# Kernel optimization log

Measured on AMD Instinct MI355X. Metric: run time of the kernel, lower is better.

Reference implementation:

```python
import jax, jax.numpy as jnp
import numpy as np

N = 200000   # nodes
E = 6400000  # directed edges (avg degree 32)
F = 128      # num_features
C = 16       # num_classes
H1, H2, H3 = 4, 4, 2  # hardcoded GCN hidden dims from the source


def setup_inputs():
    key = jax.random.key(0)
    ks = jax.random.split(key, 10)
    x = jax.random.normal(ks[0], (N, F), dtype=jnp.float32)
    edge_index = jax.random.randint(ks[1], (2, E), 0, N, dtype=jnp.int32)
    def lin(k, fin, fout):
        return jax.random.normal(k, (fin, fout), dtype=jnp.float32) / np.sqrt(fin).astype(np.float32)
    return {
        "x": x,
        "W1": lin(ks[2], F, H1),  "b1": jnp.zeros((H1,), jnp.float32),
        "W2": lin(ks[3], H1, H2), "b2": jnp.zeros((H2,), jnp.float32),
        "W3": lin(ks[4], H2, H3), "b3": jnp.zeros((H3,), jnp.float32),
        "Wc": lin(ks[5], H3, C),  "bc": jnp.zeros((C,), jnp.float32),
        "edge_index": edge_index,
    }


def _gcn_conv(h, W, b, src, dst, norm, n):
    # PyG GCNConv: linear first, then normalized scatter-add aggregation, then bias
    h = h @ W                                   # [n, fout]
    msg = h[src] * norm[:, None]                # gather + per-edge scale
    out = jax.ops.segment_sum(msg, dst, num_segments=n)
    return out + b


def reference(x, W1, b1, W2, b2, W3, b3, Wc, bc, edge_index):
    n = x.shape[0]
    # add self-loops (GCNConv default add_self_loops=True)
    loop = jnp.arange(n, dtype=edge_index.dtype)
    src = jnp.concatenate([edge_index[0], loop])
    dst = jnp.concatenate([edge_index[1], loop])
    # symmetric degree normalization: norm_e = deg(dst)^-1/2 * deg(src)^-1/2
    deg = jax.ops.segment_sum(jnp.ones(src.shape[0], dtype=x.dtype), dst, num_segments=n)
    dinv = jnp.where(deg > 0, jax.lax.rsqrt(deg), jnp.zeros_like(deg))
    norm = dinv[src] * dinv[dst]
    h = jnp.tanh(_gcn_conv(x, W1, b1, src, dst, norm, n))
    h = jnp.tanh(_gcn_conv(h, W2, b2, src, dst, norm, n))
    h = jnp.tanh(_gcn_conv(h, W3, b3, src, dst, norm, n))
    out = h @ Wc + bc
    return (out, h)
```

## Files before the change

kernel.cpp:

```cpp
#include <hip/hip_runtime.h>
#include <math.h>


#define NR 500
#define RNG 400
#define CAP 16384
#define HB 1024
#define EPT 8
#define EPB (HB * EPT)
#define SCAP 14348
#define QBLK 100
#define LROWS 32
#define LPAD 133


typedef int   vi4 __attribute__((ext_vector_type(4)));
typedef float vf4 __attribute__((ext_vector_type(4)));

static __device__ __forceinline__ int4 ldnt_i4(const int* p) {
    vi4 v = __builtin_nontemporal_load((const vi4*)p);
    return make_int4(v[0], v[1], v[2], v[3]);
}
static __device__ __forceinline__ float4 ldnt_f4(const float* p) {
    vf4 v = __builtin_nontemporal_load((const vf4*)p);
    return make_float4(v[0], v[1], v[2], v[3]);
}
static __device__ __forceinline__ void stnt_f4(float* p, float4 v) {
    vf4 w; w[0] = v.x; w[1] = v.y; w[2] = v.z; w[3] = v.w;
    __builtin_nontemporal_store(w, (vf4*)p);
}


__global__ void k_initcur(int* __restrict__ cursor, float* __restrict__ g1,
                          float* __restrict__ g2, float* __restrict__ g3, int n) {
    int t = blockIdx.x * blockDim.x + threadIdx.x;
    if (t < NR) cursor[t * 16] = t * CAP;
    if (t < 4) g1[4 * (size_t)n + t] = 0.0f;
    if (t >= 4 && t < 8) g2[4 * (size_t)n + (t - 4)] = 0.0f;
    if (t >= 8 && t < 10) g3[2 * (size_t)n + (t - 8)] = 0.0f;
}


__global__ __launch_bounds__(HB) void k_build(const int* __restrict__ src,
                                              const int* __restrict__ dst,
                                              int* __restrict__ cursor,
                                              int* __restrict__ csrp, int e) {
    __shared__ int hist[NR];
    __shared__ int start[NR + 1];
    __shared__ int gbase[NR];
    __shared__ int cur[NR];
    __shared__ int wsum[8];
    __shared__ int buf[EPB];
    __shared__ short bbin[EPB];

    int t = threadIdx.x;
    for (int i = t; i < NR; i += HB) hist[i] = 0;
    __syncthreads();

    int ds[EPT], sr[EPT];
    int base = blockIdx.x * EPB;
#pragma unroll
    for (int k = 0; k < 2; k++) {
        int idx = base + k * HB * 4 + t * 4;
        if (idx + 3 < e) {
            int4 d4 = ldnt_i4(dst + idx);
            int4 s4 = ldnt_i4(src + idx);
            ds[4 * k + 0] = d4.x; ds[4 * k + 1] = d4.y; ds[4 * k + 2] = d4.z; ds[4 * k + 3] = d4.w;
            sr[4 * k + 0] = s4.x; sr[4 * k + 1] = s4.y; sr[4 * k + 2] = s4.z; sr[4 * k + 3] = s4.w;
        } else {
#pragma unroll
            for (int j = 0; j < 4; j++) {
                int i2 = idx + j;
                if (i2 < e) { ds[4 * k + j] = dst[i2]; sr[4 * k + j] = src[i2]; }
                else ds[4 * k + j] = -1;
            }
        }
    }
#pragma unroll
    for (int k = 0; k < EPT; k++)
        if (ds[k] >= 0) atomicAdd(&hist[ds[k] / RNG], 1);
    __syncthreads();

    {
        int lane = t & 63, wv = t >> 6;
        int v = (t < NR) ? hist[t] : 0;
        int sc = v;
#pragma unroll
        for (int off = 1; off < 64; off <<= 1) {
            int u = __shfl_up(sc, off, 64);
            if (lane >= off) sc += u;
        }
        if (wv < 8 && lane == 63) wsum[wv] = sc;
        __syncthreads();
        if (t < 8) {
            int s = wsum[t];
#pragma unroll
            for (int off = 1; off < 8; off <<= 1) {
                int u = __shfl_up(s, off, 8);
                if (t >= off) s += u;
            }
            wsum[t] = s;
        }
        __syncthreads();
        int incl = sc + (wv ? wsum[wv - 1] : 0);
        if (t < NR) {
            int c = hist[t];
            int st = incl - c;
            start[t] = st;
            cur[t] = st;
            gbase[t] = c ? atomicAdd(&cursor[t * 16], c) : 0;
        }
        if (t == 0) start[NR] = wsum[7];
    }
    __syncthreads();

#pragma unroll
    for (int k = 0; k < EPT; k++) {
        if (ds[k] >= 0) {
            int bin = ds[k] / RNG;
            int p = atomicAdd(&cur[bin], 1);
            buf[p] = (sr[k] << 9) | (ds[k] - bin * RNG);
            bbin[p] = (short)bin;
        }
    }
    __syncthreads();

    int total = start[NR];
    for (int j = t; j < total; j += HB) {
        int bin = bbin[j];
        int g = gbase[bin] + (j - start[bin]);
        if (g < (bin + 1) * CAP) csrp[g] = buf[j];
    }
}


__global__ __launch_bounds__(1024) void k_sortbin(int* __restrict__ csrp,
                                                  const int* __restrict__ cursor,
                                                  int* __restrict__ split,
                                                  float* __restrict__ dinv, int n) {
    __shared__ int deg[RNG];
    __shared__ int off[RNG];
    __shared__ int cur[RNG];
    __shared__ int wsum[8];
    __shared__ int qb[5];
    __shared__ int sbuf[SCAP];
    int t = threadIdx.x, b = blockIdx.x;
    int s0 = b * CAP;
    int cnt = cursor[b * 16] - s0;
    if (cnt < 0) cnt = 0; if (cnt > CAP) cnt = CAP;

    for (int i = t; i < RNG; i += 1024) deg[i] = 0;
    __syncthreads();
    for (int j = t; j < cnt; j += 1024)
        atomicAdd(&deg[csrp[s0 + j] & 511], 1);
    __syncthreads();

    {
        int lane = t & 63, wv = t >> 6;
        int v = (t < RNG) ? deg[t] : 0;
        int sc = v;
#pragma unroll
        for (int o = 1; o < 64; o <<= 1) {
            int u = __shfl_up(sc, o, 64);
            if (lane >= o) sc += u;
        }
        if (wv < 7 && lane == 63) wsum[wv] = sc;
        __syncthreads();
        if (t < 7) {
            int s = wsum[t];
#pragma unroll
            for (int o = 1; o < 8; o <<= 1) {
                int u = __shfl_up(s, o, 8);
                if (t >= o) s += u;
            }
            wsum[t] = s;
        }
        __syncthreads();
        if (t < RNG) off[t] = sc + (wv ? wsum[wv - 1] : 0);
    }
    __syncthreads();

    if (t == 0) {
        int e0 = off[99], e1 = off[199], e2 = off[299], e3 = off[399];
        int b1 = (e0 + 3) & ~3;
        int b2 = (b1 + (e1 - e0) + 3) & ~3;
        int b3 = (b2 + (e2 - e1) + 3) & ~3;
        int b4 = (b3 + (e3 - e2) + 3) & ~3;
        qb[0] = 0; qb[1] = b1; qb[2] = b2; qb[3] = b3; qb[4] = b4;
        split[b * 4 + 0] = b1; split[b * 4 + 1] = b2;
        split[b * 4 + 2] = b3; split[b * 4 + 3] = b4;
    }
    __syncthreads();

    if (t < RNG) {
        int q = t / 100;
        int bstart = (q == 0) ? 0 : off[q * 100 - 1];
        cur[t] = (off[t] - deg[t]) - bstart + qb[q];
    }
    __syncthreads();

    for (int j = t; j < cnt; j += 1024) {
        int p = csrp[s0 + j];
        int r = atomicAdd(&cur[p & 511], 1);
        if (r < SCAP) sbuf[r] = p;
    }
    __syncthreads();

    if (t < 12) {
        int q = t / 3, sl = t - q * 3;
        int eq = off[q * 100 + 99];
        int sq = (q == 0) ? 0 : off[q * 100 - 1];
        int realend = qb[q] + (eq - sq);
        int pos = realend + sl;
        if (pos < qb[q + 1] && pos < SCAP) sbuf[pos] = (n << 9) | (q * 100);
    }
    __syncthreads();

    int lim = qb[4]; if (lim > SCAP) lim = SCAP;
    for (int j = t; j < lim; j += 1024)
        csrp[s0 + j] = sbuf[j];

    int basen = b * RNG;
    for (int i = t; i < RNG; i += 1024) {
        int node = basen + i;
        if (node < n) dinv[node] = rsqrtf(1.0f + (float)deg[i]);
    }
}


__global__ __launch_bounds__(256) void k_linear1(const float* __restrict__ x,
                                                 const float* __restrict__ W1,
                                                 const float* __restrict__ dinv,
                                                 float4* __restrict__ g1, int n) {
    __shared__ float xs[LROWS * LPAD];
    int t = threadIdx.x;
    int q = t & 7, r = t >> 3;
    int row0 = blockIdx.x * LROWS;

    float4 w[16];
#pragma unroll
    for (int i = 0; i < 16; i++) w[i] = ((const float4*)W1)[q * 16 + i];

    const float* xg = x + (size_t)row0 * 128;
    int maxI = (n - row0) * 32;
#pragma unroll
    for (int k = 0; k < 4; k++) {
        int idx = t + k * 256;
        if (idx < maxI) {
            float4 v = ldnt_f4(xg + 4 * (size_t)idx);
            int rr = idx >> 5, cc = (idx & 31) << 2;
            *(float4*)&xs[rr * LPAD + cc] = v;
        }
    }
    __syncthreads();

    float p0 = 0.f, p1 = 0.f, p2 = 0.f, p3 = 0.f;
    const float* xr = &xs[r * LPAD + q * 16];
#pragma unroll
    for (int j = 0; j < 4; j++) {
        float4 xv = *(const float4*)(xr + 4 * j);
        float4 wa = w[4 * j + 0], wb = w[4 * j + 1], wc = w[4 * j + 2], wd = w[4 * j + 3];
        p0 += xv.x * wa.x + xv.y * wb.x + xv.z * wc.x + xv.w * wd.x;
        p1 += xv.x * wa.y + xv.y * wb.y + xv.z * wc.y + xv.w * wd.y;
        p2 += xv.x * wa.z + xv.y * wb.z + xv.z * wc.z + xv.w * wd.z;
        p3 += xv.x * wa.w + xv.y * wb.w + xv.z * wc.w + xv.w * wd.w;
    }
#pragma unroll
    for (int off = 1; off < 8; off <<= 1) {
        p0 += __shfl_xor(p0, off, 64);
        p1 += __shfl_xor(p1, off, 64);
        p2 += __shfl_xor(p2, off, 64);
        p3 += __shfl_xor(p3, off, 64);
    }
    int row = row0 + r;
    if (q == 0 && row < n) {
        float dv = dinv[row];
        g1[row] = make_float4(dv * p0, dv * p1, dv * p2, dv * p3);
    }
}


#define PUSH4() { atomicAdd(&acc[cd * 5 + 0], a0); atomicAdd(&acc[cd * 5 + 1], a1); \
    atomicAdd(&acc[cd * 5 + 2], a2); atomicAdd(&acc[cd * 5 + 3], a3); }
#define EDGE4(di, gv) { int d_ = ((di) & 511) - qoff; \
    if (d_ != cd) { if (cd >= 0) PUSH4(); cd = d_; a0 = gv.x; a1 = gv.y; a2 = gv.z; a3 = gv.w; } \
    else { a0 += gv.x; a1 += gv.y; a2 += gv.z; a3 += gv.w; } }

#define EDGELOOP4P() \
    int bin = b >> 2, qq = b & 3; \
    int qoff = qq * 100; \
    int s0 = bin * CAP; \
    int lo0 = qq ? split[bin * 4 + qq - 1] : 0; \
    int hi0 = split[bin * 4 + qq]; \
    int L = hi0 - lo0; \
    int per = (((L + 255) >> 8) + 3) & ~3; \
    int lo = s0 + lo0 + t * per; \
    int hi = lo + per; int eE = s0 + hi0; if (hi > eE) hi = eE; \
    int cd = -1; float a0 = 0, a1 = 0, a2 = 0, a3 = 0; \
    int4 pA, pB; \
    float4 gA0, gA1, gA2, gA3; \
    if (lo < hi) { \
        pA = ldnt_i4(csrp + lo); \
        gA0 = gin[(unsigned)pA.x >> 9]; gA1 = gin[(unsigned)pA.y >> 9]; \
        gA2 = gin[(unsigned)pA.z >> 9]; gA3 = gin[(unsigned)pA.w >> 9]; \
        int jB = lo + 4; \
        pB = ldnt_i4(csrp + ((jB < hi) ? jB : lo)); \
    } \
    for (int j = lo; j < hi; j += 4) { \
        int4 p = pA; \
        float4 g0 = gA0, g1v = gA1, g2v = gA2, g3v = gA3; \
        int jn = j + 4; \
        pA = pB; \
        if (jn < hi) { \
            gA0 = gin[(unsigned)pA.x >> 9]; gA1 = gin[(unsigned)pA.y >> 9]; \
            gA2 = gin[(unsigned)pA.z >> 9]; gA3 = gin[(unsigned)pA.w >> 9]; \
        } \
        int jB2 = j + 8; \
        pB = ldnt_i4(csrp + ((jB2 < hi) ? jB2 : lo)); \
        EDGE4(p.x, g0); \
        EDGE4(p.y, g1v); \
        EDGE4(p.z, g2v); \
        EDGE4(p.w, g3v); \
    } \
    if (cd >= 0) PUSH4(); \
    __syncthreads();

__global__ __launch_bounds__(256) void k_bagg44s(const int* __restrict__ csrp,
                                                 const int* __restrict__ split,
                                                 const float* __restrict__ dinv,
                                                 const float4* __restrict__ gin,
                                                 float4* __restrict__ gout,
                                                 const float* __restrict__ W,
                                                 const float* __restrict__ bv, int n) {
    __shared__ float acc[QBLK * 5];
    int t = threadIdx.x, b = blockIdx.x;
    for (int i = t; i < QBLK * 5; i += 256) acc[i] = 0.0f;
    __syncthreads();
    EDGELOOP4P();
    int basen = (b >> 2) * RNG + qoff;
    for (int i = t; i < QBLK; i += 256) {
        int node = basen + i;
        if (node >= n) continue;
        float4 gs = gin[node];
        float dv = dinv[node];
        float t0 = tanhf(dv * (gs.x + acc[i * 5 + 0]) + bv[0]);
        float t1 = tanhf(dv * (gs.y + acc[i * 5 + 1]) + bv[1]);
        float t2 = tanhf(dv * (gs.z + acc[i * 5 + 2]) + bv[2]);
        float t3 = tanhf(dv * (gs.w + acc[i * 5 + 3]) + bv[3]);
        float4 o;
        o.x = dv * (t0 * W[0] + t1 * W[4] + t2 * W[8]  + t3 * W[12]);
        o.y = dv * (t0 * W[1] + t1 * W[5] + t2 * W[9]  + t3 * W[13]);
        o.z = dv * (t0 * W[2] + t1 * W[6] + t2 * W[10] + t3 * W[14]);
        o.w = dv * (t0 * W[3] + t1 * W[7] + t2 * W[11] + t3 * W[15]);
        gout[node] = o;
    }
}

__global__ __launch_bounds__(256) void k_bagg42s(const int* __restrict__ csrp,
                                                 const int* __restrict__ split,
                                                 const float* __restrict__ dinv,
                                                 const float4* __restrict__ gin,
                                                 float2* __restrict__ gout,
                                                 const float* __restrict__ W,
                                                 const float* __restrict__ bv, int n) {
    __shared__ float acc[QBLK * 5];
    int t = threadIdx.x, b = blockIdx.x;
    for (int i = t; i < QBLK * 5; i += 256) acc[i] = 0.0f;
    __syncthreads();
    EDGELOOP4P();
    int basen = (b >> 2) * RNG + qoff;
    for (int i = t; i < QBLK; i += 256) {
        int node = basen + i;
        if (node >= n) continue;
        float4 gs = gin[node];
        float dv = dinv[node];
        float t0 = tanhf(dv * (gs.x + acc[i * 5 + 0]) + bv[0]);
        float t1 = tanhf(dv * (gs.y + acc[i * 5 + 1]) + bv[1]);
        float t2 = tanhf(dv * (gs.z + acc[i * 5 + 2]) + bv[2]);
        float t3 = tanhf(dv * (gs.w + acc[i * 5 + 3]) + bv[3]);
        float h0 = t0 * W[0] + t1 * W[2] + t2 * W[4] + t3 * W[6];
        float h1 = t0 * W[1] + t1 * W[3] + t2 * W[5] + t3 * W[7];
        gout[node] = make_float2(dv * h0, dv * h1);
    }
}

#define PUSH2() { atomicAdd(&acc[cd * 3 + 0], a0); atomicAdd(&acc[cd * 3 + 1], a1); }
#define EDGE2(di, gv) { int d_ = ((di) & 511) - qoff; \
    if (d_ != cd) { if (cd >= 0) PUSH2(); cd = d_; a0 = gv.x; a1 = gv.y; } \
    else { a0 += gv.x; a1 += gv.y; } }

__global__ __launch_bounds__(256) void k_bagg2outs(const int* __restrict__ csrp,
                                                   const int* __restrict__ split,
                                                   const float* __restrict__ dinv,
                                                   const float2* __restrict__ gin,
                                                   const float* __restrict__ b3,
                                                   const float* __restrict__ Wc,
                                                   const float* __restrict__ bc,
                                                   float* __restrict__ out,
                                                   float2* __restrict__ hout, int n) {
    __shared__ float acc[QBLK * 3];
    int t = threadIdx.x, b = blockIdx.x;
    for (int i = t; i < QBLK * 3; i += 256) acc[i] = 0.0f;
    __syncthreads();
    int bin = b >> 2, qq = b & 3;
    int qoff = qq * 100;
    int s0 = bin * CAP;
    int lo0 = qq ? split[bin * 4 + qq - 1] : 0;
    int hi0 = split[bin * 4 + qq];
    int L = hi0 - lo0;
    int per = (((L + 255) >> 8) + 3) & ~3;
    int lo = s0 + lo0 + t * per;
    int hi = lo + per; int eE = s0 + hi0; if (hi > eE) hi = eE;
    int cd = -1; float a0 = 0, a1 = 0;
    int4 pA, pB;
    float2 gA0, gA1, gA2, gA3;
    if (lo < hi) {
        pA = ldnt_i4(csrp + lo);
        gA0 = gin[(unsigned)pA.x >> 9]; gA1 = gin[(unsigned)pA.y >> 9];
        gA2 = gin[(unsigned)pA.z >> 9]; gA3 = gin[(unsigned)pA.w >> 9];
        int jB = lo + 4;
        pB = ldnt_i4(csrp + ((jB < hi) ? jB : lo));
    }
    for (int j = lo; j < hi; j += 4) {
        int4 p = pA;
        float2 g0 = gA0, g1v = gA1, g2v = gA2, g3v = gA3;
        int jn = j + 4;
        pA = pB;
        if (jn < hi) {
            gA0 = gin[(unsigned)pA.x >> 9]; gA1 = gin[(unsigned)pA.y >> 9];
            gA2 = gin[(unsigned)pA.z >> 9]; gA3 = gin[(unsigned)pA.w >> 9];
        }
        int jB2 = j + 8;
        pB = ldnt_i4(csrp + ((jB2 < hi) ? jB2 : lo));
        EDGE2(p.x, g0);
        EDGE2(p.y, g1v);
        EDGE2(p.z, g2v);
        EDGE2(p.w, g3v);
    }
    if (cd >= 0) PUSH2();
    __syncthreads();
    int basen = bin * RNG + qoff;
    for (int i = t; i < QBLK; i += 256) {
        int node = basen + i;
        if (node >= n) continue;
        float2 gs = gin[node];
        float dv = dinv[node];
        float t0 = tanhf(dv * (gs.x + acc[i * 3 + 0]) + b3[0]);
        float t1 = tanhf(dv * (gs.y + acc[i * 3 + 1]) + b3[1]);
        hout[node] = make_float2(t0, t1);
        float* o = out + (size_t)node * 16;
#pragma unroll
        for (int q = 0; q < 4; q++) {
            float4 v;
            v.x = t0 * Wc[4 * q + 0] + t1 * Wc[16 + 4 * q + 0] + bc[4 * q + 0];
            v.y = t0 * Wc[4 * q + 1] + t1 * Wc[16 + 4 * q + 1] + bc[4 * q + 1];
            v.z = t0 * Wc[4 * q + 2] + t1 * Wc[16 + 4 * q + 2] + bc[4 * q + 2];
            v.w = t0 * Wc[4 * q + 3] + t1 * Wc[16 + 4 * q + 3] + bc[4 * q + 3];
            stnt_f4(o + 4 * q, v);
        }
    }
}


__global__ void k_count(const int* __restrict__ dst, int* __restrict__ cnt, int e) {
    int i = blockIdx.x * blockDim.x + threadIdx.x;
    if (i < e) atomicAdd(&cnt[dst[i]], 1);
}

__global__ void k_dinv_i(const int* __restrict__ cnt, float* __restrict__ dinv, int n) {
    int i = blockIdx.x * blockDim.x + threadIdx.x;
    if (i < n) dinv[i] = rsqrtf(1.0f + (float)cnt[i]);
}

__global__ void f_linear1(const float* __restrict__ x, const float* __restrict__ W1,
                          const float* __restrict__ dinv,
                          float* __restrict__ h, float* __restrict__ agg, int n) {
    int lane = threadIdx.x & 63;
    int wave = blockIdx.x * (blockDim.x >> 6) + (threadIdx.x >> 6);
    int nwaves = gridDim.x * (blockDim.x >> 6);
    float4 w0 = ((const float4*)W1)[2 * lane];
    float4 w1 = ((const float4*)W1)[2 * lane + 1];
    for (int row = wave; row < n; row += nwaves) {
        float2 xv = ((const float2*)(x + (size_t)row * 128))[lane];
        float p0 = xv.x * w0.x + xv.y * w1.x;
        float p1 = xv.x * w0.y + xv.y * w1.y;
        float p2 = xv.x * w0.z + xv.y * w1.z;
        float p3 = xv.x * w0.w + xv.y * w1.w;
#pragma unroll
        for (int off = 32; off; off >>= 1) {
            p0 += __shfl_xor(p0, off, 64);
            p1 += __shfl_xor(p1, off, 64);
            p2 += __shfl_xor(p2, off, 64);
            p3 += __shfl_xor(p3, off, 64);
        }
        if (lane == 0) {
            float dv = dinv[row]; float dv2 = dv * dv;
            ((float4*)h)[row] = make_float4(p0, p1, p2, p3);
            ((float4*)agg)[row] = make_float4(dv2 * p0, dv2 * p1, dv2 * p2, dv2 * p3);
        }
    }
}

__global__ void k_edge4(const int* __restrict__ src, const int* __restrict__ dst,
                        const float* __restrict__ dinv, const float* __restrict__ h,
                        float* __restrict__ agg, int e) {
    int i = blockIdx.x * blockDim.x + threadIdx.x;
    if (i >= e) return;
    int s = src[i], d = dst[i];
    float w = dinv[s] * dinv[d];
    float4 hv = ((const float4*)h)[s];
    float* a = agg + 4 * (size_t)d;
    unsafeAtomicAdd(a + 0, w * hv.x);
    unsafeAtomicAdd(a + 1, w * hv.y);
    unsafeAtomicAdd(a + 2, w * hv.z);
    unsafeAtomicAdd(a + 3, w * hv.w);
}

__global__ void k_edge2(const int* __restrict__ src, const int* __restrict__ dst,
                        const float* __restrict__ dinv, const float* __restrict__ h,
                        float* __restrict__ agg, int e) {
    int i = blockIdx.x * blockDim.x + threadIdx.x;
    if (i >= e) return;
    int s = src[i], d = dst[i];
    float w = dinv[s] * dinv[d];
    float2 hv = ((const float2*)h)[s];
    float* a = agg + 2 * (size_t)d;
    unsafeAtomicAdd(a + 0, w * hv.x);
    unsafeAtomicAdd(a + 1, w * hv.y);
}

__global__ void k_fin44(float* __restrict__ h, float* __restrict__ agg,
                        const float* __restrict__ dinv,
                        const float* __restrict__ W, const float* __restrict__ b, int n) {
    int i = blockIdx.x * blockDim.x + threadIdx.x;
    if (i >= n) return;
    float4 a = ((const float4*)agg)[i];
    float t0 = tanhf(a.x + b[0]);
    float t1 = tanhf(a.y + b[1]);
    float t2 = tanhf(a.z + b[2]);
    float t3 = tanhf(a.w + b[3]);
    float hn[4];
#pragma unroll
    for (int k = 0; k < 4; k++)
        hn[k] = t0 * W[k] + t1 * W[4 + k] + t2 * W[8 + k] + t3 * W[12 + k];
    float dv = dinv[i], dv2 = dv * dv;
    ((float4*)h)[i] = make_float4(hn[0], hn[1], hn[2], hn[3]);
    ((float4*)agg)[i] = make_float4(dv2 * hn[0], dv2 * hn[1], dv2 * hn[2], dv2 * hn[3]);
}

__global__ void k_fin42(const float* __restrict__ agg, float* __restrict__ h3,
                        float* __restrict__ agg3, const float* __restrict__ dinv,
                        const float* __restrict__ W, const float* __restrict__ b, int n) {
    int i = blockIdx.x * blockDim.x + threadIdx.x;
    if (i >= n) return;
    float4 a = ((const float4*)agg)[i];
    float t0 = tanhf(a.x + b[0]);
    float t1 = tanhf(a.y + b[1]);
    float t2 = tanhf(a.z + b[2]);
    float t3 = tanhf(a.w + b[3]);
    float h0 = t0 * W[0] + t1 * W[2] + t2 * W[4] + t3 * W[6];
    float h1 = t0 * W[1] + t1 * W[3] + t2 * W[5] + t3 * W[7];
    float dv = dinv[i], dv2 = dv * dv;
    ((float2*)h3)[i] = make_float2(h0, h1);
    ((float2*)agg3)[i] = make_float2(dv2 * h0, dv2 * h1);
}

__global__ void k_final_old(const float* __restrict__ agg3,
                            const float* __restrict__ Wc, const float* __restrict__ b3,
                            const float* __restrict__ bc,
                            float* __restrict__ out, float* __restrict__ hout, int n) {
    int i = blockIdx.x * blockDim.x + threadIdx.x;
    if (i >= n) return;
    float2 a = ((const float2*)agg3)[i];
    float t0 = tanhf(a.x + b3[0]);
    float t1 = tanhf(a.y + b3[1]);
    ((float2*)hout)[i] = make_float2(t0, t1);
    float4* o = (float4*)(out + (size_t)i * 16);
#pragma unroll
    for (int q = 0; q < 4; q++) {
        float4 v;
        v.x = t0 * Wc[4 * q + 0] + t1 * Wc[16 + 4 * q + 0] + bc[4 * q + 0];
        v.y = t0 * Wc[4 * q + 1] + t1 * Wc[16 + 4 * q + 1] + bc[4 * q + 1];
        v.z = t0 * Wc[4 * q + 2] + t1 * Wc[16 + 4 * q + 2] + bc[4 * q + 2];
        v.w = t0 * Wc[4 * q + 3] + t1 * Wc[16 + 4 * q + 3] + bc[4 * q + 3];
        o[q] = v;
    }
}


extern "C" void kernel_launch(void* const* d_in, const int* in_sizes, int n_in,
                              void* d_out, int out_size, void* d_ws, size_t ws_size,
                              hipStream_t stream) {
    const float* x   = (const float*)d_in[0];
    const float* W1  = (const float*)d_in[1];
    const float* b1  = (const float*)d_in[2];
    const float* W2  = (const float*)d_in[3];
    const float* b2  = (const float*)d_in[4];
    const float* W3  = (const float*)d_in[5];
    const float* b3  = (const float*)d_in[6];
    const float* Wc  = (const float*)d_in[7];
    const float* bc  = (const float*)d_in[8];
    const int* eidx  = (const int*)d_in[9];

    const int n = in_sizes[0] / 128;
    const int e = in_sizes[9] / 2;
    const int* src = eidx;
    const int* dst = eidx + e;

    float* out_c = (float*)d_out;
    float* out_h = (float*)d_out + 16 * (size_t)n;

    const int B = 256;
    const int gn = (n + B - 1) / B;
    const int ge = (e + B - 1) / B;
    const int nbE = (e + EPB - 1) / EPB;

    size_t nP = ((size_t)(n + 4) + 3) & ~(size_t)3;

    int* csrp    = (int*)d_ws;
    int* cursor  = csrp + (size_t)NR * CAP + 4096;
    int* split   = cursor + NR * 16;
    float* dinv  = (float*)(split + NR * 4);
    float* g1    = dinv + nP;
    float* g2    = g1 + 4 * nP;
    float* g3    = g2 + 4 * nP;
    size_t need  = (size_t)((char*)(g3 + 2 * nP) - (char*)d_ws);

    bool fast = (ws_size >= need) && (n <= NR * RNG) && (n < (1 << 18));

    if (fast) {
        k_initcur<<<(NR + 255) / 256, 256, 0, stream>>>(cursor, g1, g2, g3, n);
        k_build<<<nbE, HB, 0, stream>>>(src, dst, cursor, csrp, e);
        k_sortbin<<<NR, 1024, 0, stream>>>(csrp, cursor, split, dinv, n);

        k_linear1<<<(n + LROWS - 1) / LROWS, 256, 0, stream>>>(x, W1, dinv, (float4*)g1, n);
        k_bagg44s<<<NR * 4, 256, 0, stream>>>(csrp, split, dinv, (const float4*)g1,
                                              (float4*)g2, W2, b1, n);
        k_bagg42s<<<NR * 4, 256, 0, stream>>>(csrp, split, dinv, (const float4*)g2,
                                              (float2*)g3, W3, b2, n);
        k_bagg2outs<<<NR * 4, 256, 0, stream>>>(csrp, split, dinv, (const float2*)g3,
                                                b3, Wc, bc, out_c, (float2*)out_h, n);
    } else {
        int* fcnt   = (int*)d_ws;
        float* fdnv = (float*)d_ws + nP;
        float* h    = fdnv + nP;
        float* agg  = h + 4 * nP;
        float* h3   = agg + 4 * nP;
        float* agg3 = h3 + 2 * nP;

        hipMemsetAsync(fcnt, 0, (size_t)n * sizeof(int), stream);
        k_count<<<ge, B, 0, stream>>>(dst, fcnt, e);
        k_dinv_i<<<gn, B, 0, stream>>>(fcnt, fdnv, n);
        f_linear1<<<(n + 3) / 4, B, 0, stream>>>(x, W1, fdnv, h, agg, n);
        k_edge4<<<ge, B, 0, stream>>>(src, dst, fdnv, h, agg, e);
        k_fin44<<<gn, B, 0, stream>>>(h, agg, fdnv, W2, b1, n);
        k_edge4<<<ge, B, 0, stream>>>(src, dst, fdnv, h, agg, e);
        k_fin42<<<gn, B, 0, stream>>>(agg, h3, agg3, fdnv, W3, b2, n);
        k_edge2<<<ge, B, 0, stream>>>(src, dst, fdnv, h3, agg3, e);
        k_final_old<<<gn, B, 0, stream>>>(agg3, Wc, b3, bc, out_c, (float*)out_h, n);
    }
}
```

Before: 411.7 us.

## Fuse first linear layer into edge-binning kernel and apply dinv scaling in sortbin

The separate x@W1 kernel is removed. Extra blocks appended to the edge-binning launch now compute the unscaled product into a new h1 buffer, and k_sortbin multiplies it by dinv while writing g1. The aim is to overlap the dense 128-wide read of x with the scatter-heavy binning work and to save one launch. It also swaps all nontemporal loads and stores for plain ones and changes the linear mapping to 32 lanes per row, at the cost of an extra round trip of h1 through memory and larger shared-memory blocks being used for the linear work.

```diff
diff --git a/kernel.cpp b/kernel.cpp
--- a/kernel.cpp
+++ b/kernel.cpp
@@ -10,25 +10,7 @@
 #define EPB (HB * EPT)
 #define SCAP 14348
 #define QBLK 100
-#define LROWS 32
-#define LPAD 133
-
-
-typedef int   vi4 __attribute__((ext_vector_type(4)));
-typedef float vf4 __attribute__((ext_vector_type(4)));
-
-static __device__ __forceinline__ int4 ldnt_i4(const int* p) {
-    vi4 v = __builtin_nontemporal_load((const vi4*)p);
-    return make_int4(v[0], v[1], v[2], v[3]);
-}
-static __device__ __forceinline__ float4 ldnt_f4(const float* p) {
-    vf4 v = __builtin_nontemporal_load((const vf4*)p);
-    return make_float4(v[0], v[1], v[2], v[3]);
-}
-static __device__ __forceinline__ void stnt_f4(float* p, float4 v) {
-    vf4 w; w[0] = v.x; w[1] = v.y; w[2] = v.z; w[3] = v.w;
-    __builtin_nontemporal_store(w, (vf4*)p);
-}
+#define LINR 128
 
 
 __global__ void k_initcur(int* __restrict__ cursor, float* __restrict__ g1,
@@ -41,10 +23,14 @@
 }
 
 
-__global__ __launch_bounds__(HB) void k_build(const int* __restrict__ src,
-                                              const int* __restrict__ dst,
-                                              int* __restrict__ cursor,
-                                              int* __restrict__ csrp, int e) {
+__global__ __launch_bounds__(HB) void k_build_lin(const int* __restrict__ src,
+                                                  const int* __restrict__ dst,
+                                                  int* __restrict__ cursor,
+                                                  int* __restrict__ csrp,
+                                                  const float* __restrict__ x,
+                                                  const float* __restrict__ W1,
+                                                  float4* __restrict__ h1,
+                                                  int e, int n, int nBuild) {
     __shared__ int hist[NR];
     __shared__ int start[NR + 1];
     __shared__ int gbase[NR];
@@ -54,17 +40,47 @@
     __shared__ short bbin[EPB];
 
     int t = threadIdx.x;
+    int b = blockIdx.x;
+
+    if (b >= nBuild) {
+        int row0 = (b - nBuild) * LINR;
+        int q = t & 31, r = t >> 5;
+        float4 w0 = ((const float4*)W1)[q * 4 + 0];
+        float4 w1 = ((const float4*)W1)[q * 4 + 1];
+        float4 w2 = ((const float4*)W1)[q * 4 + 2];
+        float4 w3 = ((const float4*)W1)[q * 4 + 3];
+#pragma unroll
+        for (int rr = 0; rr < LINR / 32; rr++) {
+            int row = row0 + rr * 32 + r;
+            if (row >= n) break;
+            float4 xv = ((const float4*)(x + (size_t)row * 128))[q];
+            float p0 = xv.x * w0.x + xv.y * w1.x + xv.z * w2.x + xv.w * w3.x;
+            float p1 = xv.x * w0.y + xv.y * w1.y + xv.z * w2.y + xv.w * w3.y;
+            float p2 = xv.x * w0.z + xv.y * w1.z + xv.z * w2.z + xv.w * w3.z;
+            float p3 = xv.x * w0.w + xv.y * w1.w + xv.z * w2.w + xv.w * w3.w;
+#pragma unroll
+            for (int off = 1; off < 32; off <<= 1) {
+                p0 += __shfl_xor(p0, off, 64);
+                p1 += __shfl_xor(p1, off, 64);
+                p2 += __shfl_xor(p2, off, 64);
+                p3 += __shfl_xor(p3, off, 64);
+            }
+            if (q == 0) h1[row] = make_float4(p0, p1, p2, p3);
+        }
+        return;
+    }
+
     for (int i = t; i < NR; i += HB) hist[i] = 0;
     __syncthreads();
 
     int ds[EPT], sr[EPT];
-    int base = blockIdx.x * EPB;
+    int base = b * EPB;
 #pragma unroll
     for (int k = 0; k < 2; k++) {
         int idx = base + k * HB * 4 + t * 4;
         if (idx + 3 < e) {
-            int4 d4 = ldnt_i4(dst + idx);
-            int4 s4 = ldnt_i4(src + idx);
+            int4 d4 = *(const int4*)(dst + idx);
+            int4 s4 = *(const int4*)(src + idx);
             ds[4 * k + 0] = d4.x; ds[4 * k + 1] = d4.y; ds[4 * k + 2] = d4.z; ds[4 * k + 3] = d4.w;
             sr[4 * k + 0] = s4.x; sr[4 * k + 1] = s4.y; sr[4 * k + 2] = s4.z; sr[4 * k + 3] = s4.w;
         } else {
@@ -137,7 +153,9 @@
 __global__ __launch_bounds__(1024) void k_sortbin(int* __restrict__ csrp,
                                                   const int* __restrict__ cursor,
                                                   int* __restrict__ split,
-                                                  float* __restrict__ dinv, int n) {
+                                                  float* __restrict__ dinv,
+                                                  const float4* __restrict__ h1,
+                                                  float4* __restrict__ g1, int n) {
     __shared__ int deg[RNG];
     __shared__ int off[RNG];
     __shared__ int cur[RNG];
@@ -223,59 +241,12 @@
     int basen = b * RNG;
     for (int i = t; i < RNG; i += 1024) {
         int node = basen + i;
-        if (node < n) dinv[node] = rsqrtf(1.0f + (float)deg[i]);
-    }
-}
-
-
-__global__ __launch_bounds__(256) void k_linear1(const float* __restrict__ x,
-                                                 const float* __restrict__ W1,
-                                                 const float* __restrict__ dinv,
-                                                 float4* __restrict__ g1, int n) {
-    __shared__ float xs[LROWS * LPAD];
-    int t = threadIdx.x;
-    int q = t & 7, r = t >> 3;
-    int row0 = blockIdx.x * LROWS;
-
-    float4 w[16];
-#pragma unroll
-    for (int i = 0; i < 16; i++) w[i] = ((const float4*)W1)[q * 16 + i];
-
-    const float* xg = x + (size_t)row0 * 128;
-    int maxI = (n - row0) * 32;
-#pragma unroll
-    for (int k = 0; k < 4; k++) {
-        int idx = t + k * 256;
-        if (idx < maxI) {
-            float4 v = ldnt_f4(xg + 4 * (size_t)idx);
-            int rr = idx >> 5, cc = (idx & 31) << 2;
-            *(float4*)&xs[rr * LPAD + cc] = v;
-        }
-    }
-    __syncthreads();
-
-    float p0 = 0.f, p1 = 0.f, p2 = 0.f, p3 = 0.f;
-    const float* xr = &xs[r * LPAD + q * 16];
-#pragma unroll
-    for (int j = 0; j < 4; j++) {
-        float4 xv = *(const float4*)(xr + 4 * j);
-        float4 wa = w[4 * j + 0], wb = w[4 * j + 1], wc = w[4 * j + 2], wd = w[4 * j + 3];
-        p0 += xv.x * wa.x + xv.y * wb.x + xv.z * wc.x + xv.w * wd.x;
-        p1 += xv.x * wa.y + xv.y * wb.y + xv.z * wc.y + xv.w * wd.y;
-        p2 += xv.x * wa.z + xv.y * wb.z + xv.z * wc.z + xv.w * wd.z;
-        p3 += xv.x * wa.w + xv.y * wb.w + xv.z * wc.w + xv.w * wd.w;
-    }
-#pragma unroll
-    for (int off = 1; off < 8; off <<= 1) {
-        p0 += __shfl_xor(p0, off, 64);
-        p1 += __shfl_xor(p1, off, 64);
-        p2 += __shfl_xor(p2, off, 64);
-        p3 += __shfl_xor(p3, off, 64);
-    }
-    int row = row0 + r;
-    if (q == 0 && row < n) {
-        float dv = dinv[row];
-        g1[row] = make_float4(dv * p0, dv * p1, dv * p2, dv * p3);
+        if (node < n) {
+            float dv = rsqrtf(1.0f + (float)deg[i]);
+            dinv[node] = dv;
+            float4 hv = h1[node];
+            g1[node] = make_float4(dv * hv.x, dv * hv.y, dv * hv.z, dv * hv.w);
+        }
     }
 }
 
@@ -300,11 +271,11 @@
     int4 pA, pB; \
     float4 gA0, gA1, gA2, gA3; \
     if (lo < hi) { \
-        pA = ldnt_i4(csrp + lo); \
+        pA = *(const int4*)(csrp + lo); \
         gA0 = gin[(unsigned)pA.x >> 9]; gA1 = gin[(unsigned)pA.y >> 9]; \
         gA2 = gin[(unsigned)pA.z >> 9]; gA3 = gin[(unsigned)pA.w >> 9]; \
         int jB = lo + 4; \
-        pB = ldnt_i4(csrp + ((jB < hi) ? jB : lo)); \
+        pB = *(const int4*)(csrp + ((jB < hi) ? jB : lo)); \
     } \
     for (int j = lo; j < hi; j += 4) { \
         int4 p = pA; \
@@ -316,7 +287,7 @@
             gA2 = gin[(unsigned)pA.z >> 9]; gA3 = gin[(unsigned)pA.w >> 9]; \
         } \
         int jB2 = j + 8; \
-        pB = ldnt_i4(csrp + ((jB2 < hi) ? jB2 : lo)); \
+        pB = *(const int4*)(csrp + ((jB2 < hi) ? jB2 : lo)); \
         EDGE4(p.x, g0); \
         EDGE4(p.y, g1v); \
         EDGE4(p.z, g2v); \
@@ -415,11 +386,11 @@
     int4 pA, pB;
     float2 gA0, gA1, gA2, gA3;
     if (lo < hi) {
-        pA = ldnt_i4(csrp + lo);
+        pA = *(const int4*)(csrp + lo);
         gA0 = gin[(unsigned)pA.x >> 9]; gA1 = gin[(unsigned)pA.y >> 9];
         gA2 = gin[(unsigned)pA.z >> 9]; gA3 = gin[(unsigned)pA.w >> 9];
         int jB = lo + 4;
-        pB = ldnt_i4(csrp + ((jB < hi) ? jB : lo));
+        pB = *(const int4*)(csrp + ((jB < hi) ? jB : lo));
     }
     for (int j = lo; j < hi; j += 4) {
         int4 p = pA;
@@ -431,7 +402,7 @@
             gA2 = gin[(unsigned)pA.z >> 9]; gA3 = gin[(unsigned)pA.w >> 9];
         }
         int jB2 = j + 8;
-        pB = ldnt_i4(csrp + ((jB2 < hi) ? jB2 : lo));
+        pB = *(const int4*)(csrp + ((jB2 < hi) ? jB2 : lo));
         EDGE2(p.x, g0);
         EDGE2(p.y, g1v);
         EDGE2(p.z, g2v);
@@ -448,7 +419,7 @@
         float t0 = tanhf(dv * (gs.x + acc[i * 3 + 0]) + b3[0]);
         float t1 = tanhf(dv * (gs.y + acc[i * 3 + 1]) + b3[1]);
         hout[node] = make_float2(t0, t1);
-        float* o = out + (size_t)node * 16;
+        float4* o = (float4*)(out + (size_t)node * 16);
 #pragma unroll
         for (int q = 0; q < 4; q++) {
             float4 v;
@@ -456,7 +427,7 @@
             v.y = t0 * Wc[4 * q + 1] + t1 * Wc[16 + 4 * q + 1] + bc[4 * q + 1];
             v.z = t0 * Wc[4 * q + 2] + t1 * Wc[16 + 4 * q + 2] + bc[4 * q + 2];
             v.w = t0 * Wc[4 * q + 3] + t1 * Wc[16 + 4 * q + 3] + bc[4 * q + 3];
-            stnt_f4(o + 4 * q, v);
+            o[q] = v;
         }
     }
 }
@@ -614,6 +585,7 @@
     const int gn = (n + B - 1) / B;
     const int ge = (e + B - 1) / B;
     const int nbE = (e + EPB - 1) / EPB;
+    const int nbL = (n + LINR - 1) / LINR;
 
     size_t nP = ((size_t)(n + 4) + 3) & ~(size_t)3;
 
@@ -621,7 +593,8 @@
     int* cursor  = csrp + (size_t)NR * CAP + 4096;
     int* split   = cursor + NR * 16;
     float* dinv  = (float*)(split + NR * 4);
-    float* g1    = dinv + nP;
+    float* h1    = dinv + nP;
+    float* g1    = h1 + 4 * nP;
     float* g2    = g1 + 4 * nP;
     float* g3    = g2 + 4 * nP;
     size_t need  = (size_t)((char*)(g3 + 2 * nP) - (char*)d_ws);
@@ -630,10 +603,11 @@
 
     if (fast) {
         k_initcur<<<(NR + 255) / 256, 256, 0, stream>>>(cursor, g1, g2, g3, n);
-        k_build<<<nbE, HB, 0, stream>>>(src, dst, cursor, csrp, e);
-        k_sortbin<<<NR, 1024, 0, stream>>>(csrp, cursor, split, dinv, n);
-
-        k_linear1<<<(n + LROWS - 1) / LROWS, 256, 0, stream>>>(x, W1, dinv, (float4*)g1, n);
+        k_build_lin<<<nbE + nbL, HB, 0, stream>>>(src, dst, cursor, csrp,
+                                                  x, W1, (float4*)h1, e, n, nbE);
+        k_sortbin<<<NR, 1024, 0, stream>>>(csrp, cursor, split, dinv,
+                                           (const float4*)h1, (float4*)g1, n);
+
         k_bagg44s<<<NR * 4, 256, 0, stream>>>(csrp, split, dinv, (const float4*)g1,
                                               (float4*)g2, W2, b1, n);
         k_bagg42s<<<NR * 4, 256, 0, stream>>>(csrp, split, dinv, (const float4*)g2,
```

New measurement: 356.3 us. 13.4% less time.
